# Kernel optimization log

Hardware: AMD Instinct MI355X
Metric: run time of the kernel (lower is better)

## Reference

```python
import jax, jax.numpy as jnp
import numpy as np

T, N = 8192, 4096
DT = 0.01


def setup_inputs() -> dict:
    key = jax.random.key(0)
    k_in, k_tau, k_b = jax.random.split(key, 3)
    inp = jax.random.normal(k_in, (T, N), dtype=jnp.float32)
    tau = jax.random.uniform(k_tau, (N,), dtype=jnp.float32)  # forward clamps to >= dt
    bias = jax.random.normal(k_b, (N,), dtype=jnp.float32)
    return {"input": inp, "tau": tau, "bias": bias}


def reference(input, tau, bias):
    # s_{t+1} = s_t + (dt/tau) * (x_t - s_t), s_0 = input[0]; out_t = s_{t+1} + bias
    dt = jnp.asarray(DT, input.dtype)
    a = dt / jnp.clip(tau, dt, None)  # [N], per-channel leak rate

    def step(s, x_t):
        s_next = s + a * (x_t - s)
        return s_next, s_next

    _, states = jax.lax.scan(step, input[0], input)  # [T, N]
    out = states + bias  # [T, N]
    # torch.cat of T vectors of shape [N] along dim 0 -> flat [T*N]
    return out.reshape(-1)
```

## Files before the change

kernel.cpp:

```cpp
#include <hip/hip_runtime.h>

#define DT 0.01f

typedef float f32x4 __attribute__((ext_vector_type(4)));


__global__ __launch_bounds__(256) void fol_pass1_L16(
        const float* __restrict__ in, const float* __restrict__ tau,
        float* __restrict__ B, int N4) {
    const int chunk = blockIdx.y;
    const int ch4 = blockIdx.x * 256 + threadIdx.x;
    if (ch4 >= N4) return;

    const float4* p = reinterpret_cast<const float4*>(in) + (size_t)chunk * 16 * N4 + ch4;
    float4 x[16];
    #pragma unroll
    for (int t = 0; t < 16; ++t) x[t] = p[(size_t)t * N4];

    const float4 tv = reinterpret_cast<const float4*>(tau)[ch4];
    const float ax = DT / fmaxf(tv.x, DT), ay = DT / fmaxf(tv.y, DT),
                az = DT / fmaxf(tv.z, DT), aw = DT / fmaxf(tv.w, DT);
    const float qx = 1.f - ax, qy = 1.f - ay, qz = 1.f - az, qw = 1.f - aw;

    float sx = 0.f, sy = 0.f, sz = 0.f, sw = 0.f;
    #pragma unroll
    for (int t = 0; t < 16; ++t) {
        sx = fmaf(qx, sx, ax * x[t].x);
        sy = fmaf(qy, sy, ay * x[t].y);
        sz = fmaf(qz, sz, az * x[t].z);
        sw = fmaf(qw, sw, aw * x[t].w);
    }
    reinterpret_cast<float4*>(B)[(size_t)chunk * N4 + ch4] = make_float4(sx, sy, sz, sw);
}

__global__ __launch_bounds__(256) void fol_pass2_pipe(
        const float* __restrict__ in, const float* __restrict__ tau,
        float* __restrict__ B, int N, int C, int L) {
    const int ch = blockIdx.x * 256 + threadIdx.x;
    if (ch >= N) return;
    const float a = DT / fmaxf(tau[ch], DT);
    const float q = 1.f - a;
    float qL = 1.f, b = q;
    int e = L;
    while (e) { if (e & 1) qL *= b; b *= b; e >>= 1; }

    float S = in[ch];

    constexpr int BATCH = 32;
    float x[BATCH], xn[BATCH];
    #pragma unroll
    for (int j = 0; j < BATCH; ++j) x[j] = B[(size_t)j * N + ch];

    for (int cb = 0; cb < C; cb += BATCH) {
        const int nb = cb + BATCH;
        if (nb < C) {
            #pragma unroll
            for (int j = 0; j < BATCH; ++j) xn[j] = B[(size_t)(nb + j) * N + ch];
        }
        #pragma unroll
        for (int j = 0; j < BATCH; ++j) {
            B[(size_t)(cb + j) * N + ch] = S;
            S = fmaf(qL, S, x[j]);
        }
        #pragma unroll
        for (int j = 0; j < BATCH; ++j) x[j] = xn[j];
    }
}

__global__ __launch_bounds__(256) void fol_pass3_L16(
        const float* __restrict__ in, const float* __restrict__ tau,
        const float* __restrict__ bias, const float* __restrict__ S,
        float* __restrict__ out, int N4) {
    const int chunk = blockIdx.y;
    const int ch4 = blockIdx.x * 256 + threadIdx.x;
    if (ch4 >= N4) return;

    const float4* p = reinterpret_cast<const float4*>(in) + (size_t)chunk * 16 * N4 + ch4;
    float4 x[16];
    #pragma unroll
    for (int t = 0; t < 16; ++t) x[t] = p[(size_t)t * N4];

    const float4 tv = reinterpret_cast<const float4*>(tau)[ch4];
    const float4 bv = reinterpret_cast<const float4*>(bias)[ch4];
    const float ax = DT / fmaxf(tv.x, DT), ay = DT / fmaxf(tv.y, DT),
                az = DT / fmaxf(tv.z, DT), aw = DT / fmaxf(tv.w, DT);
    const float qx = 1.f - ax, qy = 1.f - ay, qz = 1.f - az, qw = 1.f - aw;

    const float4 sv = reinterpret_cast<const float4*>(S)[(size_t)chunk * N4 + ch4];
    float sx = sv.x, sy = sv.y, sz = sv.z, sw = sv.w;

    f32x4* o = reinterpret_cast<f32x4*>(out) + (size_t)chunk * 16 * N4 + ch4;
    #pragma unroll
    for (int t = 0; t < 16; ++t) {
        sx = fmaf(qx, sx, ax * x[t].x);
        sy = fmaf(qy, sy, ay * x[t].y);
        sz = fmaf(qz, sz, az * x[t].z);
        sw = fmaf(qw, sw, aw * x[t].w);
        f32x4 ov; ov.x = sx + bv.x; ov.y = sy + bv.y; ov.z = sz + bv.z; ov.w = sw + bv.w;
        __builtin_nontemporal_store(ov, &o[(size_t)t * N4]);
    }
}


__global__ void fol_pass1_gen(const float* __restrict__ in, const float* __restrict__ tau,
                              float* __restrict__ B, int N, int L) {
    const int chunk = blockIdx.y;
    const int N4 = N >> 2;
    const int ch4 = blockIdx.x * blockDim.x + threadIdx.x;
    if (ch4 >= N4) return;
    const float4 tv = reinterpret_cast<const float4*>(tau)[ch4];
    const float ax = DT / fmaxf(tv.x, DT), ay = DT / fmaxf(tv.y, DT),
                az = DT / fmaxf(tv.z, DT), aw = DT / fmaxf(tv.w, DT);
    const float qx = 1.f - ax, qy = 1.f - ay, qz = 1.f - az, qw = 1.f - aw;
    float sx = 0.f, sy = 0.f, sz = 0.f, sw = 0.f;
    const float4* p = reinterpret_cast<const float4*>(in) + (size_t)chunk * L * N4 + ch4;
    #pragma unroll 8
    for (int t = 0; t < L; ++t) {
        const float4 x = p[(size_t)t * N4];
        sx = fmaf(qx, sx, ax * x.x);
        sy = fmaf(qy, sy, ay * x.y);
        sz = fmaf(qz, sz, az * x.z);
        sw = fmaf(qw, sw, aw * x.w);
    }
    reinterpret_cast<float4*>(B)[(size_t)chunk * N4 + ch4] = make_float4(sx, sy, sz, sw);
}

__global__ void fol_pass3_gen(const float* __restrict__ in, const float* __restrict__ tau,
                              const float* __restrict__ bias, const float* __restrict__ S,
                              float* __restrict__ out, int N, int L) {
    const int chunk = blockIdx.y;
    const int N4 = N >> 2;
    const int ch4 = blockIdx.x * blockDim.x + threadIdx.x;
    if (ch4 >= N4) return;
    const float4 tv = reinterpret_cast<const float4*>(tau)[ch4];
    const float4 bv = reinterpret_cast<const float4*>(bias)[ch4];
    const float ax = DT / fmaxf(tv.x, DT), ay = DT / fmaxf(tv.y, DT),
                az = DT / fmaxf(tv.z, DT), aw = DT / fmaxf(tv.w, DT);
    const float qx = 1.f - ax, qy = 1.f - ay, qz = 1.f - az, qw = 1.f - aw;
    const float4 sv = reinterpret_cast<const float4*>(S)[(size_t)chunk * N4 + ch4];
    float sx = sv.x, sy = sv.y, sz = sv.z, sw = sv.w;
    const float4* p = reinterpret_cast<const float4*>(in) + (size_t)chunk * L * N4 + ch4;
    float4*       o = reinterpret_cast<float4*>(out)      + (size_t)chunk * L * N4 + ch4;
    #pragma unroll 8
    for (int t = 0; t < L; ++t) {
        const float4 x = p[(size_t)t * N4];
        sx = fmaf(qx, sx, ax * x.x);
        sy = fmaf(qy, sy, ay * x.y);
        sz = fmaf(qz, sz, az * x.z);
        sw = fmaf(qw, sw, aw * x.w);
        o[(size_t)t * N4] = make_float4(sx + bv.x, sy + bv.y, sz + bv.z, sw + bv.w);
    }
}

__global__ void fol_naive(const float* __restrict__ in, const float* __restrict__ tau,
                          const float* __restrict__ bias, float* __restrict__ out,
                          int N, int T) {
    const int ch = blockIdx.x * blockDim.x + threadIdx.x;
    if (ch >= N) return;
    const float a = DT / fmaxf(tau[ch], DT);
    const float q = 1.f - a;
    const float b = bias[ch];
    float s = in[ch];
    for (int t = 0; t < T; ++t) {
        const float x = in[(size_t)t * N + ch];
        s = fmaf(q, s, a * x);
        out[(size_t)t * N + ch] = s + b;
    }
}

extern "C" void kernel_launch(void* const* d_in, const int* in_sizes, int n_in,
                              void* d_out, int out_size, void* d_ws, size_t ws_size,
                              hipStream_t stream) {
    const float* in   = (const float*)d_in[0];
    const float* tau  = (const float*)d_in[1];
    const float* bias = (const float*)d_in[2];
    float* out = (float*)d_out;

    const int N = in_sizes[1];
    const int T = in_sizes[0] / N;

    const bool vec_ok = (N % 4 == 0);
    float* B = (float*)d_ws;

    if (vec_ok && T == 8192 && ((size_t)512 * N * sizeof(float)) <= ws_size) {
        const int C = 512, L = 16, N4 = N / 4;
        const dim3 blk(256);
        const dim3 g13((N4 + 255) / 256, C);
        fol_pass1_L16<<<g13, blk, 0, stream>>>(in, tau, B, N4);
        fol_pass2_pipe<<<dim3((N + 255) / 256), blk, 0, stream>>>(in, tau, B, N, C, L);
        fol_pass3_L16<<<g13, blk, 0, stream>>>(in, tau, bias, B, out, N4);
        return;
    }

    int C = 512;
    while (C > 1 && (((size_t)C * N * sizeof(float)) > ws_size || (T % C) != 0 || (C % 32) != 0)) C >>= 1;
    if (C >= 32 && vec_ok && ((size_t)C * N * sizeof(float)) <= ws_size) {
        const int L = T / C, N4 = N / 4;
        const dim3 blk(256);
        const dim3 g13((N4 + 255) / 256, C);
        fol_pass1_gen<<<g13, blk, 0, stream>>>(in, tau, B, N, L);
        fol_pass2_pipe<<<dim3((N + 255) / 256), blk, 0, stream>>>(in, tau, B, N, C, L);
        fol_pass3_gen<<<g13, blk, 0, stream>>>(in, tau, bias, B, out, N, L);
        return;
    }

    fol_naive<<<dim3((N + 255) / 256), dim3(256), 0, stream>>>(in, tau, bias, out, N, T);
}
```

Measured before the change: 271.6 us.

## Fuse three scan passes into one cooperative kernel with grid syncs

Replaces the three separate launches (chunk reduce, carry propagation, chunk rescan) with a single cooperative kernel that uses grid-wide syncs between phases. It also lengthens chunks to 32 steps, halving the number of chunks the serial carry pass must walk and shrinking the workspace. This removes launch gaps and kernel-boundary drain, but adds grid barrier cost and leaves most blocks idle during the serial middle phase. A non-cooperative fallback path is kept.

```diff
diff --git a/kernel.cpp b/kernel.cpp
--- a/kernel.cpp
+++ b/kernel.cpp
@@ -1,8 +1,105 @@
 #include <hip/hip_runtime.h>
+#include <hip/hip_cooperative_groups.h>
+
+namespace cg = cooperative_groups;
 
 #define DT 0.01f
 
 typedef float f32x4 __attribute__((ext_vector_type(4)));
+
+__global__ __launch_bounds__(256, 4) void fol_fused(
+        const float* __restrict__ in, const float* __restrict__ tau,
+        const float* __restrict__ bias, float* __restrict__ out,
+        float* __restrict__ B, int N4, int C, int L, int nSlice, int nChBlk) {
+    cg::grid_group grid = cg::this_grid();
+
+    const int tid = threadIdx.x;
+    const int c  = blockIdx.x / nSlice;
+    const int sl = blockIdx.x % nSlice;
+    const int ch4 = sl * 256 + tid;
+
+    const float4 tv = reinterpret_cast<const float4*>(tau)[ch4];
+    const float ax = DT / fmaxf(tv.x, DT), ay = DT / fmaxf(tv.y, DT),
+                az = DT / fmaxf(tv.z, DT), aw = DT / fmaxf(tv.w, DT);
+    const float qx = 1.f - ax, qy = 1.f - ay, qz = 1.f - az, qw = 1.f - aw;
+
+    {
+        const float4* p = reinterpret_cast<const float4*>(in) + (size_t)c * L * N4 + ch4;
+        float sx = 0.f, sy = 0.f, sz = 0.f, sw = 0.f;
+        float4 x[8];
+        for (int h = 0; h < L; h += 8) {
+            #pragma unroll
+            for (int j = 0; j < 8; ++j) x[j] = p[(size_t)(h + j) * N4];
+            #pragma unroll
+            for (int j = 0; j < 8; ++j) {
+                sx = fmaf(qx, sx, ax * x[j].x);
+                sy = fmaf(qy, sy, ay * x[j].y);
+                sz = fmaf(qz, sz, az * x[j].z);
+                sw = fmaf(qw, sw, aw * x[j].w);
+            }
+        }
+        reinterpret_cast<float4*>(B)[(size_t)c * N4 + ch4] = make_float4(sx, sy, sz, sw);
+    }
+
+    grid.sync();
+
+    if ((int)blockIdx.x < nChBlk) {
+        const int ch = blockIdx.x * 256 + tid;
+        const int N = N4 * 4;
+        const float a = DT / fmaxf(tau[ch], DT);
+        const float q = 1.f - a;
+        float qL = 1.f, bb = q;
+        int e = L;
+        while (e) { if (e & 1) qL *= bb; bb *= bb; e >>= 1; }
+
+        float S = in[ch];
+
+        constexpr int BATCH = 16;
+        float x[BATCH], xn[BATCH];
+        #pragma unroll
+        for (int j = 0; j < BATCH; ++j) x[j] = B[(size_t)j * N + ch];
+
+        for (int cb = 0; cb < C; cb += BATCH) {
+            const int nb = cb + BATCH;
+            if (nb < C) {
+                #pragma unroll
+                for (int j = 0; j < BATCH; ++j) xn[j] = B[(size_t)(nb + j) * N + ch];
+            }
+            #pragma unroll
+            for (int j = 0; j < BATCH; ++j) {
+                B[(size_t)(cb + j) * N + ch] = S;
+                S = fmaf(qL, S, x[j]);
+            }
+            #pragma unroll
+            for (int j = 0; j < BATCH; ++j) x[j] = xn[j];
+        }
+    }
+
+    grid.sync();
+
+    {
+        const float4 bv = reinterpret_cast<const float4*>(bias)[ch4];
+        const float4 sv = reinterpret_cast<const float4*>(B)[(size_t)c * N4 + ch4];
+        float sx = sv.x, sy = sv.y, sz = sv.z, sw = sv.w;
+
+        const float4* p = reinterpret_cast<const float4*>(in) + (size_t)c * L * N4 + ch4;
+        f32x4*       o = reinterpret_cast<f32x4*>(out)        + (size_t)c * L * N4 + ch4;
+        float4 x[8];
+        for (int h = 0; h < L; h += 8) {
+            #pragma unroll
+            for (int j = 0; j < 8; ++j) x[j] = p[(size_t)(h + j) * N4];
+            #pragma unroll
+            for (int j = 0; j < 8; ++j) {
+                sx = fmaf(qx, sx, ax * x[j].x);
+                sy = fmaf(qy, sy, ay * x[j].y);
+                sz = fmaf(qz, sz, az * x[j].z);
+                sw = fmaf(qw, sw, aw * x[j].w);
+                f32x4 ov; ov.x = sx + bv.x; ov.y = sy + bv.y; ov.z = sz + bv.z; ov.w = sw + bv.w;
+                __builtin_nontemporal_store(ov, &o[(size_t)(h + j) * N4]);
+            }
+        }
+    }
+}
 
 
 __global__ __launch_bounds__(256) void fol_pass1_L16(
@@ -11,17 +108,14 @@
     const int chunk = blockIdx.y;
     const int ch4 = blockIdx.x * 256 + threadIdx.x;
     if (ch4 >= N4) return;
-
     const float4* p = reinterpret_cast<const float4*>(in) + (size_t)chunk * 16 * N4 + ch4;
     float4 x[16];
     #pragma unroll
     for (int t = 0; t < 16; ++t) x[t] = p[(size_t)t * N4];
-
     const float4 tv = reinterpret_cast<const float4*>(tau)[ch4];
     const float ax = DT / fmaxf(tv.x, DT), ay = DT / fmaxf(tv.y, DT),
                 az = DT / fmaxf(tv.z, DT), aw = DT / fmaxf(tv.w, DT);
     const float qx = 1.f - ax, qy = 1.f - ay, qz = 1.f - az, qw = 1.f - aw;
-
     float sx = 0.f, sy = 0.f, sz = 0.f, sw = 0.f;
     #pragma unroll
     for (int t = 0; t < 16; ++t) {
@@ -43,14 +137,11 @@
     float qL = 1.f, b = q;
     int e = L;
     while (e) { if (e & 1) qL *= b; b *= b; e >>= 1; }
-
     float S = in[ch];
-
     constexpr int BATCH = 32;
     float x[BATCH], xn[BATCH];
     #pragma unroll
     for (int j = 0; j < BATCH; ++j) x[j] = B[(size_t)j * N + ch];
-
     for (int cb = 0; cb < C; cb += BATCH) {
         const int nb = cb + BATCH;
         if (nb < C) {
@@ -74,21 +165,17 @@
     const int chunk = blockIdx.y;
     const int ch4 = blockIdx.x * 256 + threadIdx.x;
     if (ch4 >= N4) return;
-
     const float4* p = reinterpret_cast<const float4*>(in) + (size_t)chunk * 16 * N4 + ch4;
     float4 x[16];
     #pragma unroll
     for (int t = 0; t < 16; ++t) x[t] = p[(size_t)t * N4];
-
     const float4 tv = reinterpret_cast<const float4*>(tau)[ch4];
     const float4 bv = reinterpret_cast<const float4*>(bias)[ch4];
     const float ax = DT / fmaxf(tv.x, DT), ay = DT / fmaxf(tv.y, DT),
                 az = DT / fmaxf(tv.z, DT), aw = DT / fmaxf(tv.w, DT);
     const float qx = 1.f - ax, qy = 1.f - ay, qz = 1.f - az, qw = 1.f - aw;
-
     const float4 sv = reinterpret_cast<const float4*>(S)[(size_t)chunk * N4 + ch4];
     float sx = sv.x, sy = sv.y, sz = sv.z, sw = sv.w;
-
     f32x4* o = reinterpret_cast<f32x4*>(out) + (size_t)chunk * 16 * N4 + ch4;
     #pragma unroll
     for (int t = 0; t < 16; ++t) {
@@ -98,57 +185,6 @@
         sw = fmaf(qw, sw, aw * x[t].w);
         f32x4 ov; ov.x = sx + bv.x; ov.y = sy + bv.y; ov.z = sz + bv.z; ov.w = sw + bv.w;
         __builtin_nontemporal_store(ov, &o[(size_t)t * N4]);
-    }
-}
-
-
-__global__ void fol_pass1_gen(const float* __restrict__ in, const float* __restrict__ tau,
-                              float* __restrict__ B, int N, int L) {
-    const int chunk = blockIdx.y;
-    const int N4 = N >> 2;
-    const int ch4 = blockIdx.x * blockDim.x + threadIdx.x;
-    if (ch4 >= N4) return;
-    const float4 tv = reinterpret_cast<const float4*>(tau)[ch4];
-    const float ax = DT / fmaxf(tv.x, DT), ay = DT / fmaxf(tv.y, DT),
-                az = DT / fmaxf(tv.z, DT), aw = DT / fmaxf(tv.w, DT);
-    const float qx = 1.f - ax, qy = 1.f - ay, qz = 1.f - az, qw = 1.f - aw;
-    float sx = 0.f, sy = 0.f, sz = 0.f, sw = 0.f;
-    const float4* p = reinterpret_cast<const float4*>(in) + (size_t)chunk * L * N4 + ch4;
-    #pragma unroll 8
-    for (int t = 0; t < L; ++t) {
-        const float4 x = p[(size_t)t * N4];
-        sx = fmaf(qx, sx, ax * x.x);
-        sy = fmaf(qy, sy, ay * x.y);
-        sz = fmaf(qz, sz, az * x.z);
-        sw = fmaf(qw, sw, aw * x.w);
-    }
-    reinterpret_cast<float4*>(B)[(size_t)chunk * N4 + ch4] = make_float4(sx, sy, sz, sw);
-}
-
-__global__ void fol_pass3_gen(const float* __restrict__ in, const float* __restrict__ tau,
-                              const float* __restrict__ bias, const float* __restrict__ S,
-                              float* __restrict__ out, int N, int L) {
-    const int chunk = blockIdx.y;
-    const int N4 = N >> 2;
-    const int ch4 = blockIdx.x * blockDim.x + threadIdx.x;
-    if (ch4 >= N4) return;
-    const float4 tv = reinterpret_cast<const float4*>(tau)[ch4];
-    const float4 bv = reinterpret_cast<const float4*>(bias)[ch4];
-    const float ax = DT / fmaxf(tv.x, DT), ay = DT / fmaxf(tv.y, DT),
-                az = DT / fmaxf(tv.z, DT), aw = DT / fmaxf(tv.w, DT);
-    const float qx = 1.f - ax, qy = 1.f - ay, qz = 1.f - az, qw = 1.f - aw;
-    const float4 sv = reinterpret_cast<const float4*>(S)[(size_t)chunk * N4 + ch4];
-    float sx = sv.x, sy = sv.y, sz = sv.z, sw = sv.w;
-    const float4* p = reinterpret_cast<const float4*>(in) + (size_t)chunk * L * N4 + ch4;
-    float4*       o = reinterpret_cast<float4*>(out)      + (size_t)chunk * L * N4 + ch4;
-    #pragma unroll 8
-    for (int t = 0; t < L; ++t) {
-        const float4 x = p[(size_t)t * N4];
-        sx = fmaf(qx, sx, ax * x.x);
-        sy = fmaf(qy, sy, ay * x.y);
-        sz = fmaf(qz, sz, az * x.z);
-        sw = fmaf(qw, sw, aw * x.w);
-        o[(size_t)t * N4] = make_float4(sx + bv.x, sy + bv.y, sz + bv.z, sw + bv.w);
     }
 }
 
@@ -168,20 +204,10 @@
     }
 }
 
-extern "C" void kernel_launch(void* const* d_in, const int* in_sizes, int n_in,
-                              void* d_out, int out_size, void* d_ws, size_t ws_size,
-                              hipStream_t stream) {
-    const float* in   = (const float*)d_in[0];
-    const float* tau  = (const float*)d_in[1];
-    const float* bias = (const float*)d_in[2];
-    float* out = (float*)d_out;
-
-    const int N = in_sizes[1];
-    const int T = in_sizes[0] / N;
-
+static void launch_fallback(const float* in, const float* tau, const float* bias,
+                            float* out, float* B, int N, int T, size_t ws_size,
+                            hipStream_t stream) {
     const bool vec_ok = (N % 4 == 0);
-    float* B = (float*)d_ws;
-
     if (vec_ok && T == 8192 && ((size_t)512 * N * sizeof(float)) <= ws_size) {
         const int C = 512, L = 16, N4 = N / 4;
         const dim3 blk(256);
@@ -191,18 +217,41 @@
         fol_pass3_L16<<<g13, blk, 0, stream>>>(in, tau, bias, B, out, N4);
         return;
     }
-
-    int C = 512;
-    while (C > 1 && (((size_t)C * N * sizeof(float)) > ws_size || (T % C) != 0 || (C % 32) != 0)) C >>= 1;
-    if (C >= 32 && vec_ok && ((size_t)C * N * sizeof(float)) <= ws_size) {
-        const int L = T / C, N4 = N / 4;
-        const dim3 blk(256);
-        const dim3 g13((N4 + 255) / 256, C);
-        fol_pass1_gen<<<g13, blk, 0, stream>>>(in, tau, B, N, L);
-        fol_pass2_pipe<<<dim3((N + 255) / 256), blk, 0, stream>>>(in, tau, B, N, C, L);
-        fol_pass3_gen<<<g13, blk, 0, stream>>>(in, tau, bias, B, out, N, L);
-        return;
-    }
-
     fol_naive<<<dim3((N + 255) / 256), dim3(256), 0, stream>>>(in, tau, bias, out, N, T);
 }
+
+extern "C" void kernel_launch(void* const* d_in, const int* in_sizes, int n_in,
+                              void* d_out, int out_size, void* d_ws, size_t ws_size,
+                              hipStream_t stream) {
+    const float* in   = (const float*)d_in[0];
+    const float* tau  = (const float*)d_in[1];
+    const float* bias = (const float*)d_in[2];
+    float* out = (float*)d_out;
+    float* B   = (float*)d_ws;
+
+    const int N = in_sizes[1];
+    const int T = in_sizes[0] / N;
+
+    const int L = 32;
+    if (N % 1024 == 0 && T % L == 0) {
+        int N4 = N / 4;
+        int C = T / L;
+        int nSlice = N4 / 256;
+        int nChBlk = N / 256;
+        const bool fits = ((size_t)C * N * sizeof(float) <= ws_size) &&
+                          (C % 16 == 0) && ((size_t)C * nSlice <= 1024) &&
+                          (nChBlk <= C * nSlice);
+        if (fits) {
+            void* args[] = {(void*)&in, (void*)&tau, (void*)&bias, (void*)&out,
+                            (void*)&B, (void*)&N4, (void*)&C, (void*)&L,
+                            (void*)&nSlice, (void*)&nChBlk};
+            hipError_t err = hipLaunchCooperativeKernel(
+                reinterpret_cast<void*>(fol_fused), dim3(C * nSlice), dim3(256),
+                args, 0, stream);
+            if (err == hipSuccess) return;
+            (void)hipGetLastError();
+        }
+    }
+
+    launch_fallback(in, tau, bias, out, B, N, T, ws_size, stream);
+}
```

Measured after the change: 493.4 us. 1.82x slower.
